# Kernel tuning notes

Hardware: AMD Instinct MI355X
Metric: run time of the kernel (lower is better)

Reference implementation:

```python
import jax, jax.numpy as jnp
import numpy as np

B, D, S, L = 4, 512, 2048, 8921

def setup_inputs() -> dict:
    key = jax.random.key(0)
    ks = jax.random.split(key, 4)
    H = jax.random.normal(ks[0], (B, D, S), dtype=jnp.float32)
    # 1x1 conv weights collapse to [out, in] matrices (xavier-ish scale)
    Wk = jax.random.normal(ks[1], (D, D), dtype=jnp.float32) * (1.0 / np.sqrt(D))
    Wv = jax.random.normal(ks[2], (D, D), dtype=jnp.float32) * (1.0 / np.sqrt(D))
    bk = jnp.full((D,), 0.01, dtype=jnp.float32)
    bv = jnp.full((D,), 0.01, dtype=jnp.float32)
    Q = jax.random.normal(ks[3], (L, D), dtype=jnp.float32) * 0.02
    return {"H": H, "Wk": Wk, "bk": bk, "Wv": Wv, "bv": bv, "Q": Q}

def reference(H, Wk, bk, Wv, bv, Q):
    # K/V: 1x1 Conv1d over channels + bias, ELU, permute(0,2,1) -> [B,S,D]
    K = jax.nn.elu(jnp.einsum('od,bds->bso', Wk, H) + bk)
    V = jax.nn.elu(jnp.einsum('od,bds->bso', Wv, H) + bv)
    # TargetAttention: energy E = Q K^T -> [B,L,S], softmax over seq (scale=False)
    E = jnp.einsum('ld,bsd->bls', Q, K)
    A = jax.nn.softmax(E, axis=-1)
    C = jnp.einsum('bls,bsd->bld', A, V)  # [B, L, D]
    return (C, A)
```

## Files before the change

### kernel.cpp

```cpp
#include <hip/hip_runtime.h>
#include <math.h>

#define Bn 4
#define Dn 512
#define Sn 2048
#define Ln 8921
#define Lpad 8960

typedef short bf16x8 __attribute__((ext_vector_type(8)));
typedef float f32x4 __attribute__((ext_vector_type(4)));

__device__ __forceinline__ float elu1(float x) {
    return x > 0.f ? x : expm1f(x);
}

__device__ __forceinline__ unsigned f2bf(float f) {
    unsigned u = __float_as_uint(f);
    u += 0x7FFFu + ((u >> 16) & 1u);
    return u >> 16;
}
__device__ __forceinline__ unsigned pack2(float a, float b) {
    return f2bf(a) | (f2bf(b) << 16);
}
__device__ __forceinline__ unsigned pack_bf_trunc(float lo, float hi) {
    return __builtin_amdgcn_perm(__float_as_uint(hi), __float_as_uint(lo), 0x07060302u);
}
__device__ __forceinline__ void gld_lds16(const void* g, void* l) {
    __builtin_amdgcn_global_load_lds((const __attribute__((address_space(1))) int*)g,
                                     (__attribute__((address_space(3))) int*)l, 16, 0, 0);
}

__global__ __launch_bounds__(256) void h_transpose(const float* __restrict__ H,
                                                   short* __restrict__ Ht) {
    int b = blockIdx.z;
    int s0 = blockIdx.x * 64, d0 = blockIdx.y * 64;
    __shared__ float tile[64][65];
    int t = threadIdx.x;
    int r = t >> 4, c4 = (t & 15) * 4;
    const float* Hb = H + (size_t)b * Dn * Sn;
#pragma unroll
    for (int i = 0; i < 4; ++i) {
        float4 v = *(const float4*)(Hb + (size_t)(d0 + i * 16 + r) * Sn + s0 + c4);
        *(float4*)&tile[i * 16 + r][c4] = v;
    }
    __syncthreads();
#pragma unroll
    for (int i = 0; i < 4; ++i) {
        int srow = i * 16 + r;
        float v0 = tile[c4 + 0][srow], v1 = tile[c4 + 1][srow];
        float v2 = tile[c4 + 2][srow], v3 = tile[c4 + 3][srow];
        uint2 o = make_uint2(pack2(v0, v1), pack2(v2, v3));
        *(uint2*)(Ht + ((size_t)b * Sn + s0 + srow) * Dn + d0 + c4) = o;
    }
}

__global__ __launch_bounds__(256) void f32_to_bf16(const float* __restrict__ src,
                                                   short* __restrict__ dst, int n8) {
    int id = blockIdx.x * 256 + threadIdx.x;
    if (id >= n8) return;
    const float* s = src + (size_t)id * 8;
    float4 a = *(const float4*)s;
    float4 b = *(const float4*)(s + 4);
    uint4 o = {pack2(a.x, a.y), pack2(a.z, a.w), pack2(b.x, b.y), pack2(b.z, b.w)};
    *(uint4*)(dst + (size_t)id * 8) = o;
}

__global__ __launch_bounds__(256) void q_to_bf16(const float* __restrict__ Q,
                                                 short* __restrict__ Qb) {
    int id = blockIdx.x * 256 + threadIdx.x;
    int row = id >> 6, c = (id & 63) * 8;
    uint4 o = {0, 0, 0, 0};
    if (row < Ln) {
        const float* src = Q + (size_t)row * Dn + c;
        float4 a = *(const float4*)src;
        float4 b = *(const float4*)(src + 4);
        o.x = pack2(a.x, a.y); o.y = pack2(a.z, a.w);
        o.z = pack2(b.x, b.y); o.w = pack2(b.z, b.w);
    }
    *(uint4*)(Qb + (size_t)id * 8) = o;
}

template <int OUT_BF16, int EPI>
__global__ __launch_bounds__(256) void gemm_nt(const short* __restrict__ A,
                                               const short* __restrict__ B,
                                               const float* __restrict__ bias,
                                               void* __restrict__ Out,
                                               int K, int lda, int ldb, int ldo,
                                               int mmax,
                                               long bA, long bB, long bO) {
    const int b  = blockIdx.z;
    const int n0 = blockIdx.x * 128;
    const int m0 = blockIdx.y * 128;
    __shared__ short lA[128 * 32];
    __shared__ short lB[128 * 32];
    const int t = threadIdx.x;
    const int lane = t & 63, w = t >> 6;
    const int wm = (w & 1) * 64, wn = (w >> 1) * 64;
    const int quad = lane >> 4, l15 = lane & 15;
    f32x4 acc[4][4] = {};
    const short* Ab = A + (size_t)bA * b + (size_t)m0 * lda;
    const short* Bb = B + (size_t)bB * b + (size_t)n0 * ldb;
    const int sr = t >> 2, ss = (t & 3) * 8;

    for (int k0 = 0; k0 < K; k0 += 32) {
        gld_lds16(Ab + (size_t)sr * lda + k0 + ss,        lA + t * 8);
        gld_lds16(Ab + (size_t)(sr + 64) * lda + k0 + ss, lA + 2048 + t * 8);
        gld_lds16(Bb + (size_t)sr * ldb + k0 + ss,        lB + t * 8);
        gld_lds16(Bb + (size_t)(sr + 64) * ldb + k0 + ss, lB + 2048 + t * 8);
        __syncthreads();
        bf16x8 af[4], bfr[4];
#pragma unroll
        for (int i = 0; i < 4; ++i)
            af[i] = *(const bf16x8*)&lA[(wm + i * 16 + l15) * 32 + quad * 8];
#pragma unroll
        for (int j = 0; j < 4; ++j)
            bfr[j] = *(const bf16x8*)&lB[(wn + j * 16 + l15) * 32 + quad * 8];
#pragma unroll
        for (int i = 0; i < 4; ++i)
#pragma unroll
            for (int j = 0; j < 4; ++j)
                acc[i][j] = __builtin_amdgcn_mfma_f32_16x16x32_bf16(af[i], bfr[j], acc[i][j], 0, 0, 0);
        __syncthreads();
    }

#pragma unroll
    for (int i = 0; i < 4; ++i) {
        int mb = m0 + wm + i * 16 + quad * 4;
#pragma unroll
        for (int r = 0; r < 4; ++r) {
            int m = mb + r;
            if (m < mmax) {
                float bm = (EPI == 2) ? bias[m] : 0.f;
#pragma unroll
                for (int j = 0; j < 4; ++j) {
                    int col = n0 + wn + j * 16 + l15;
                    float v = acc[i][j][r];
                    if (EPI == 1) v = elu1(v + bias[col]);
                    if (EPI == 2) v = elu1(v + bm);
                    if (OUT_BF16)
                        ((short*)Out)[(size_t)bO * b + (size_t)m * ldo + col] = (short)f2bf(v);
                    else
                        ((float*)Out)[(size_t)bO * b + (size_t)m * ldo + col] = v;
                }
            }
        }
    }
}

__global__ __launch_bounds__(256) void softmax_bf16(short* __restrict__ EA,
                                                    float* __restrict__ Aout) {
    int row = blockIdx.x;
    int b = row / Ln, l = row - b * Ln;
    short* pe = EA + ((size_t)b * Lpad + l) * Sn;
    float* pa = Aout + (size_t)row * Sn;
    int t = threadIdx.x;
    uint4 raw = *(const uint4*)(pe + t * 8);
    unsigned pw[4] = {raw.x, raw.y, raw.z, raw.w};
    float v[8];
#pragma unroll
    for (int q = 0; q < 4; ++q) {
        v[2 * q]     = __uint_as_float(pw[q] << 16);
        v[2 * q + 1] = __uint_as_float(pw[q] & 0xFFFF0000u);
    }
    float m = v[0];
#pragma unroll
    for (int i = 1; i < 8; ++i) m = fmaxf(m, v[i]);
#pragma unroll
    for (int off = 32; off >= 1; off >>= 1) m = fmaxf(m, __shfl_xor(m, off));
    __shared__ float sm[4], ssum[4];
    int lane = t & 63, wv = t >> 6;
    if (lane == 0) sm[wv] = m;
    __syncthreads();
    m = fmaxf(fmaxf(sm[0], sm[1]), fmaxf(sm[2], sm[3]));
    float s = 0.f;
#pragma unroll
    for (int i = 0; i < 8; ++i) {
        v[i] = expf(v[i] - m);
        s += v[i];
    }
#pragma unroll
    for (int off = 32; off >= 1; off >>= 1) s += __shfl_xor(s, off);
    if (lane == 0) ssum[wv] = s;
    __syncthreads();
    s = ssum[0] + ssum[1] + ssum[2] + ssum[3];
    float inv = 1.f / s;
#pragma unroll
    for (int i = 0; i < 8; ++i) v[i] *= inv;
    float4 o0 = {v[0], v[1], v[2], v[3]};
    float4 o1 = {v[4], v[5], v[6], v[7]};
    *(float4*)(pa + t * 8)     = o0;
    *(float4*)(pa + t * 8 + 4) = o1;
    uint4 ob = {pack2(v[0], v[1]), pack2(v[2], v[3]), pack2(v[4], v[5]), pack2(v[6], v[7])};
    *(uint4*)(pe + t * 8) = ob;
}

__global__ __launch_bounds__(256) void softmax_f32(float* __restrict__ E) {
    size_t row = blockIdx.x;
    float* p = E + row * (size_t)Sn;
    int t = threadIdx.x;
    float4 u0 = *(const float4*)(p + t * 8);
    float4 u1 = *(const float4*)(p + t * 8 + 4);
    float v[8] = {u0.x, u0.y, u0.z, u0.w, u1.x, u1.y, u1.z, u1.w};
    float m = v[0];
#pragma unroll
    for (int i = 1; i < 8; ++i) m = fmaxf(m, v[i]);
#pragma unroll
    for (int off = 32; off >= 1; off >>= 1) m = fmaxf(m, __shfl_xor(m, off));
    __shared__ float sm[4], ssum[4];
    int lane = t & 63, wv = t >> 6;
    if (lane == 0) sm[wv] = m;
    __syncthreads();
    m = fmaxf(fmaxf(sm[0], sm[1]), fmaxf(sm[2], sm[3]));
    float s = 0.f;
#pragma unroll
    for (int i = 0; i < 8; ++i) {
        v[i] = expf(v[i] - m);
        s += v[i];
    }
#pragma unroll
    for (int off = 32; off >= 1; off >>= 1) s += __shfl_xor(s, off);
    if (lane == 0) ssum[wv] = s;
    __syncthreads();
    s = ssum[0] + ssum[1] + ssum[2] + ssum[3];
    float inv = 1.f / s;
#pragma unroll
    for (int i = 0; i < 8; ++i) v[i] *= inv;
    float4 o0 = {v[0], v[1], v[2], v[3]};
    float4 o1 = {v[4], v[5], v[6], v[7]};
    *(float4*)(p + t * 8)     = o0;
    *(float4*)(p + t * 8 + 4) = o1;
}

__global__ __launch_bounds__(256) void c_mfma_f32(const float* __restrict__ A,
                                                  const short* __restrict__ Vt,
                                                  float* __restrict__ C) {
    const int b  = blockIdx.z;
    const int n0 = blockIdx.x * 128;
    const int m0 = blockIdx.y * 128;
    __shared__ short lA[128 * 32];
    __shared__ short lB[128 * 32];
    const int t = threadIdx.x;
    const int lane = t & 63, w = t >> 6;
    const int wm = (w & 1) * 64, wn = (w >> 1) * 64;
    const int quad = lane >> 4, l15 = lane & 15;
    f32x4 acc[4][4] = {};
    const float* Ab = A + (size_t)b * Ln * Sn;
    const short* Bb = Vt + (size_t)b * Dn * Sn + (size_t)n0 * Sn;
    const int ar = t >> 1, ah = (t & 1) * 16;
    const int br = t >> 2, bs = (t & 3) * 8;
    const int am = m0 + ar;
    const bool arow_ok = (am < Ln);
    const float* asrc0 = Ab + (size_t)am * Sn + ah;

    for (int s0 = 0; s0 < Sn; s0 += 32) {
        gld_lds16(Bb + (size_t)br * Sn + s0 + bs,        lB + t * 8);
        gld_lds16(Bb + (size_t)(br + 64) * Sn + s0 + bs, lB + 2048 + t * 8);
        unsigned p[8] = {0, 0, 0, 0, 0, 0, 0, 0};
        if (arow_ok) {
            const float* src = asrc0 + s0;
            float4 f0 = *(const float4*)(src);
            float4 f1 = *(const float4*)(src + 4);
            float4 f2 = *(const float4*)(src + 8);
            float4 f3 = *(const float4*)(src + 12);
            p[0] = pack_bf_trunc(f0.x, f0.y); p[1] = pack_bf_trunc(f0.z, f0.w);
            p[2] = pack_bf_trunc(f1.x, f1.y); p[3] = pack_bf_trunc(f1.z, f1.w);
            p[4] = pack_bf_trunc(f2.x, f2.y); p[5] = pack_bf_trunc(f2.z, f2.w);
            p[6] = pack_bf_trunc(f3.x, f3.y); p[7] = pack_bf_trunc(f3.z, f3.w);
        }
        *(uint4*)&lA[ar * 32 + ah]     = *(uint4*)&p[0];
        *(uint4*)&lA[ar * 32 + ah + 8] = *(uint4*)&p[4];
        __syncthreads();
        bf16x8 af[4], bfr[4];
#pragma unroll
        for (int i = 0; i < 4; ++i)
            af[i] = *(const bf16x8*)&lA[(wm + i * 16 + l15) * 32 + quad * 8];
#pragma unroll
        for (int j = 0; j < 4; ++j)
            bfr[j] = *(const bf16x8*)&lB[(wn + j * 16 + l15) * 32 + quad * 8];
#pragma unroll
        for (int i = 0; i < 4; ++i)
#pragma unroll
            for (int j = 0; j < 4; ++j)
                acc[i][j] = __builtin_amdgcn_mfma_f32_16x16x32_bf16(af[i], bfr[j], acc[i][j], 0, 0, 0);
        __syncthreads();
    }

#pragma unroll
    for (int i = 0; i < 4; ++i) {
        int mb = m0 + wm + i * 16 + quad * 4;
#pragma unroll
        for (int r = 0; r < 4; ++r) {
            int m = mb + r;
            if (m < Ln) {
                float* dst = C + (size_t)b * Ln * Dn + (size_t)m * Dn + n0 + wn;
#pragma unroll
                for (int j = 0; j < 4; ++j) dst[j * 16 + l15] = acc[i][j][r];
            }
        }
    }
}

extern "C" void kernel_launch(void* const* d_in, const int* in_sizes, int n_in,
                              void* d_out, int out_size, void* d_ws, size_t ws_size,
                              hipStream_t stream) {
    const float* H  = (const float*)d_in[0];
    const float* Wk = (const float*)d_in[1];
    const float* bk = (const float*)d_in[2];
    const float* Wv = (const float*)d_in[3];
    const float* bv = (const float*)d_in[4];
    const float* Q  = (const float*)d_in[5];

    float* out  = (float*)d_out;
    float* Cout = out;
    float* Aout = out + (size_t)Bn * Ln * Dn;

    short* Vt  = (short*)d_ws;
    short* Kb  = Vt + (size_t)Bn * Dn * Sn;
    short* Qb  = Kb + (size_t)Bn * Sn * Dn;
    short* EAb = Qb + (size_t)Lpad * Dn;
    short* Ht  = EAb;
    short* Wkb = Ht + (size_t)Bn * Sn * Dn;
    short* Wvb = Wkb + (size_t)Dn * Dn;

    size_t need_primary =
        2 * ((size_t)Bn * Dn * Sn + (size_t)Bn * Sn * Dn + (size_t)Lpad * Dn +
             (size_t)Bn * Lpad * Sn);
    bool big = ws_size >= need_primary;

    h_transpose<<<dim3(Sn / 64, Dn / 64, Bn), 256, 0, stream>>>(H, Ht);
    f32_to_bf16<<<(Dn * Dn / 8 + 255) / 256, 256, 0, stream>>>(Wk, Wkb, Dn * Dn / 8);
    f32_to_bf16<<<(Dn * Dn / 8 + 255) / 256, 256, 0, stream>>>(Wv, Wvb, Dn * Dn / 8);
    q_to_bf16<<<(Lpad * 64) / 256, 256, 0, stream>>>(Q, Qb);

    gemm_nt<1, 1><<<dim3(Dn / 128, Sn / 128, Bn), 256, 0, stream>>>(
        Ht, Wkb, bk, Kb, Dn, Dn, Dn, Dn, Sn,
        (long)Sn * Dn, 0L, (long)Sn * Dn);

    gemm_nt<1, 2><<<dim3(Sn / 128, Dn / 128, Bn), 256, 0, stream>>>(
        Wvb, Ht, bv, Vt, Dn, Dn, Dn, Sn, Dn,
        0L, (long)Sn * Dn, (long)Dn * Sn);

    if (big) {
        gemm_nt<1, 0><<<dim3(Sn / 128, Lpad / 128, Bn), 256, 0, stream>>>(
            Qb, Kb, nullptr, EAb, Dn, Dn, Dn, Sn, Ln,
            0L, (long)Sn * Dn, (long)Lpad * Sn);
        softmax_bf16<<<Bn * Ln, 256, 0, stream>>>(EAb, Aout);
        gemm_nt<0, 0><<<dim3(Dn / 128, Lpad / 128, Bn), 256, 0, stream>>>(
            EAb, Vt, nullptr, Cout, Sn, Sn, Sn, Dn, Ln,
            (long)Lpad * Sn, (long)Dn * Sn, (long)Ln * Dn);
    } else {
        gemm_nt<0, 0><<<dim3(Sn / 128, Lpad / 128, Bn), 256, 0, stream>>>(
            Qb, Kb, nullptr, Aout, Dn, Dn, Dn, Sn, Ln,
            0L, (long)Sn * Dn, (long)Ln * Sn);
        softmax_f32<<<Bn * Ln, 256, 0, stream>>>(Aout);
        c_mfma_f32<<<dim3(Dn / 128, Lpad / 128, Bn), 256, 0, stream>>>(Aout, Vt, Cout);
    }
}
```

Before: 739.5 us.

## Use 256x256-tile, 4-stage pipelined bf16 GEMM for attention matmuls

Adds a new GEMM kernel with 512 threads per block and 256x256 output tiles. Operands are staged into a 4-slot LDS ring with direct global-to-LDS loads and a swizzled layout, and waits are set by explicit vmcnt. It replaces the 128x128 GEMM for both the energy (QK^T) and context (AV) products. The aim is more data reuse per LDS load and better latency hiding, at the cost of 128KB of LDS per block, lower occupancy, and a small grid for the AV GEMM (280 blocks) that may leave CUs idle.

```diff
diff --git a/kernel.cpp b/kernel.cpp
--- a/kernel.cpp
+++ b/kernel.cpp
@@ -147,6 +147,111 @@
     }
 }
 
+template <int OUT_BF16>
+__global__ __launch_bounds__(512, 2) void gemm_nt256(const short* __restrict__ A,
+                                                     const short* __restrict__ B,
+                                                     void* __restrict__ Out,
+                                                     int K, int lda, int ldb, int ldo,
+                                                     int mmax,
+                                                     long bA, long bB, long bO) {
+    const int b  = blockIdx.z;
+    const int n0 = blockIdx.x * 256;
+    const int m0 = blockIdx.y * 256;
+    __shared__ short lds[65536];
+    const int t = threadIdx.x;
+    const int lane = t & 63, w = t >> 6;
+    const int wm = w >> 2, wn = w & 3;
+    const int quad = lane >> 4, l15 = lane & 15;
+    const int xr = (l15 >> 1) & 3;
+
+    const short* Ab = A + (size_t)bA * b + (size_t)m0 * lda;
+    const short* Bb = B + (size_t)bB * b + (size_t)n0 * ldb;
+
+    const short* srcA[2]; const short* srcB[2];
+    int dstA[2], dstB[2];
+#pragma unroll
+    for (int i = 0; i < 2; ++i) {
+        int p = i * 512 + t;
+        int g = p ^ ((p >> 3) & 3);
+        int row = g >> 2, q = g & 3;
+        srcA[i] = Ab + (size_t)row * lda + q * 8;
+        srcB[i] = Bb + (size_t)row * ldb + q * 8;
+        dstA[i] = p * 8;
+        dstB[i] = 8192 + p * 8;
+    }
+
+    int offA[8], offB[4];
+#pragma unroll
+    for (int m = 0; m < 8; ++m) {
+        int c = (wm * 128 + m * 16 + l15) * 4 + quad;
+        offA[m] = (c ^ xr) * 8;
+    }
+#pragma unroll
+    for (int j = 0; j < 4; ++j) {
+        int c = (wn * 64 + j * 16 + l15) * 4 + quad;
+        offB[j] = 8192 + (c ^ xr) * 8;
+    }
+
+    f32x4 acc[8][4] = {};
+    const int NK = K >> 5;
+
+    auto STAGE = [&](int kt) {
+        const int slot = (kt & 3) * 16384;
+        const int ko = kt * 32;
+#pragma unroll
+        for (int i = 0; i < 2; ++i) {
+            gld_lds16(srcA[i] + ko, &lds[slot + dstA[i]]);
+            gld_lds16(srcB[i] + ko, &lds[slot + dstB[i]]);
+        }
+    };
+
+    STAGE(0); STAGE(1); STAGE(2);
+
+    for (int k = 0; k < NK; ++k) {
+        asm volatile("s_waitcnt lgkmcnt(0)" ::: "memory");
+        if (k < NK - 2)
+            asm volatile("s_waitcnt vmcnt(8)" ::: "memory");
+        else if (k == NK - 2)
+            asm volatile("s_waitcnt vmcnt(4)" ::: "memory");
+        else
+            asm volatile("s_waitcnt vmcnt(0)" ::: "memory");
+        __builtin_amdgcn_s_barrier();
+        asm volatile("" ::: "memory");
+        if (k + 3 < NK) STAGE(k + 3);
+        const short* sl = &lds[(k & 3) * 16384];
+        bf16x8 af[8], bfv[4];
+#pragma unroll
+        for (int m = 0; m < 8; ++m) af[m] = *(const bf16x8*)(sl + offA[m]);
+#pragma unroll
+        for (int j = 0; j < 4; ++j) bfv[j] = *(const bf16x8*)(sl + offB[j]);
+#pragma unroll
+        for (int m = 0; m < 8; ++m)
+#pragma unroll
+            for (int j = 0; j < 4; ++j)
+                acc[m][j] = __builtin_amdgcn_mfma_f32_16x16x32_bf16(af[m], bfv[j], acc[m][j], 0, 0, 0);
+    }
+
+#pragma unroll
+    for (int m = 0; m < 8; ++m) {
+        int mb = m0 + wm * 128 + m * 16 + quad * 4;
+#pragma unroll
+        for (int r = 0; r < 4; ++r) {
+            int mm = mb + r;
+            if (mm < mmax) {
+#pragma unroll
+                for (int j = 0; j < 4; ++j) {
+                    int col = n0 + wn * 64 + j * 16 + l15;
+                    float v = acc[m][j][r];
+                    if (OUT_BF16)
+                        ((short*)Out)[(size_t)bO * b + (size_t)mm * ldo + col] = (short)f2bf(v);
+                    else
+                        ((float*)Out)[(size_t)bO * b + (size_t)mm * ldo + col] = v;
+                }
+            }
+        }
+    }
+}
+
 __global__ __launch_bounds__(256) void softmax_bf16(short* __restrict__ EA,
                                                     float* __restrict__ Aout) {
     int row = blockIdx.x;
@@ -341,12 +446,12 @@
         0L, (long)Sn * Dn, (long)Dn * Sn);
 
     if (big) {
-        gemm_nt<1, 0><<<dim3(Sn / 128, Lpad / 128, Bn), 256, 0, stream>>>(
-            Qb, Kb, nullptr, EAb, Dn, Dn, Dn, Sn, Ln,
+        gemm_nt256<1><<<dim3(Sn / 256, Lpad / 256, Bn), 512, 0, stream>>>(
+            Qb, Kb, EAb, Dn, Dn, Dn, Sn, Lpad,
             0L, (long)Sn * Dn, (long)Lpad * Sn);
         softmax_bf16<<<Bn * Ln, 256, 0, stream>>>(EAb, Aout);
-        gemm_nt<0, 0><<<dim3(Dn / 128, Lpad / 128, Bn), 256, 0, stream>>>(
-            EAb, Vt, nullptr, Cout, Sn, Sn, Sn, Dn, Ln,
+        gemm_nt256<0><<<dim3(Dn / 256, Lpad / 256, Bn), 512, 0, stream>>>(
+            EAb, Vt, Cout, Sn, Sn, Sn, Dn, Ln,
             (long)Lpad * Sn, (long)Dn * Sn, (long)Ln * Dn);
     } else {
         gemm_nt<0, 0><<<dim3(Sn / 128, Lpad / 128, Bn), 256, 0, stream>>>(
```

Result: faster. 720.9 us (-2.5%).
